# Optimization experiments

Hardware: AMD Instinct MI355X
Metric: run time of the kernel (lower is better)

The kernel has to match this reference:

```python
import jax, jax.numpy as jnp
import numpy as np

EPS = 1e-7
MIN_NORM = 1e-15
PROJ_EPS = 1e-5
NEG_SLOPE = 0.2
HEADS = 4


def artanh(x):
    return jnp.arctanh(jnp.clip(x, -1.0 + EPS, 1.0 - EPS))


def _norm(x):
    return jnp.clip(jnp.linalg.norm(x, axis=-1, keepdims=True), MIN_NORM)


def proj(x):
    # project onto Poincare ball (c=1)
    n = _norm(x)
    maxn = 1.0 - PROJ_EPS
    return jnp.where(n > maxn, x / n * maxn, x)


def expmap0(u):
    n = _norm(u)
    return jnp.tanh(n) * u / n


def logmap0(x):
    n = _norm(x)
    return artanh(n) * x / n


def mobius_add(x, y):
    x2 = jnp.sum(x * x, axis=-1, keepdims=True)
    y2 = jnp.sum(y * y, axis=-1, keepdims=True)
    xy = jnp.sum(x * y, axis=-1, keepdims=True)
    num = (1.0 + 2.0 * xy + y2) * x + (1.0 - x2) * y
    den = 1.0 + 2.0 * xy + x2 * y2
    return num / jnp.clip(den, MIN_NORM)


def pdist(x, y):
    # Poincare distance, c=1 -> [...,] scalar
    ma = mobius_add(-x, y)
    return 2.0 * artanh(jnp.linalg.norm(ma, axis=-1))


def mobius_scalar_mul(r, x):
    n = _norm(x)
    return jnp.tanh(r * artanh(n)) * x / n


def mobius_matvec(W, x):
    # x: [N,din], W: [dout,din]
    mx = x @ W.T
    n_x = _norm(x)
    n_mx = _norm(mx)
    return jnp.tanh(n_mx / n_x * artanh(n_x)) * mx / n_mx


def segment_softmax(logits, seg, num_segments):
    m = jax.ops.segment_max(logits, seg, num_segments=num_segments)
    m = jnp.where(jnp.isfinite(m), m, 0.0)
    e = jnp.exp(logits - m[seg])
    s = jax.ops.segment_sum(e, seg, num_segments=num_segments)
    return e / (s[seg] + 1e-16)


def setup_inputs() -> dict:
    N, E, D = 50000, 500000, 128
    H = HEADS
    Dh = D // H
    ks = jax.random.split(jax.random.key(0), 12)
    # edges without self-loops (reference re-adds them, mirroring remove/add_self_loops)
    src = jax.random.randint(ks[0], (E,), 0, N)
    off = jax.random.randint(ks[1], (E,), 1, N)
    dst = (src + off) % N
    edge_index = jnp.stack([src, dst]).astype(jnp.int32)
    x_e = 0.1 * jax.random.normal(ks[2], (N, D), dtype=jnp.float32)
    x_h = proj(expmap0(0.05 * jax.random.normal(ks[3], (N, D), dtype=jnp.float32)))
    sc = 1.0 / np.sqrt(D)
    W_e = sc * jax.random.normal(ks[4], (D, D), dtype=jnp.float32)
    b_lin_e = jnp.zeros((D,), jnp.float32)
    att_e = 0.1 * jax.random.normal(ks[5], (1, H, 2 * Dh), dtype=jnp.float32)
    b_e = jnp.zeros((D,), jnp.float32)
    W_h = sc * jax.random.normal(ks[6], (D, D), dtype=jnp.float32)
    b_lin_h = jnp.zeros((D,), jnp.float32)
    att_h = 0.1 * jax.random.normal(ks[7], (1, H, 2 * Dh), dtype=jnp.float32)
    b_h = jnp.zeros((D,), jnp.float32)
    att_hf = 0.1 * jax.random.normal(ks[8], (1, 1), dtype=jnp.float32)
    att_ef = 0.1 * jax.random.normal(ks[9], (1, 1), dtype=jnp.float32)
    return {"x_e": x_e, "x_h": x_h, "edge_index": edge_index,
            "W_e": W_e, "b_lin_e": b_lin_e, "att_e": att_e, "b_e": b_e,
            "W_h": W_h, "b_lin_h": b_lin_h, "att_h": att_h, "b_h": b_h,
            "att_hf": att_hf, "att_ef": att_ef}


def reference(x_e, x_h, edge_index, W_e, b_lin_e, att_e, b_e,
              W_h, b_lin_h, att_h, b_h, att_hf, att_ef):
    N, D = x_e.shape
    H = HEADS
    Dh = att_e.shape[-1] // 2
    loop = jnp.arange(N, dtype=edge_index.dtype)
    src = jnp.concatenate([edge_index[0], loop])  # j (source)
    dst = jnp.concatenate([edge_index[1], loop])  # i (target, softmax segment)

    # ---- Euclidean GAT branch (GATConv) ----
    xe = (x_e @ W_e.T + b_lin_e).reshape(N, H, Dh)
    a_i = jnp.sum(xe * att_e[:, :, :Dh], axis=-1)  # [N,H] target part
    a_j = jnp.sum(xe * att_e[:, :, Dh:], axis=-1)  # [N,H] source part
    alpha = jax.nn.leaky_relu(a_i[dst] + a_j[src], NEG_SLOPE)  # [E',H]
    alpha = segment_softmax(alpha, dst, N)
    agg = jax.ops.segment_sum(xe[src] * alpha[:, :, None], dst, num_segments=N)
    e_out = jax.nn.relu(agg.reshape(N, H * Dh) + b_e)

    # ---- Hyperbolic GAT branch (HGATConv with HypLinear) ----
    mv = proj(mobius_matvec(W_h, x_h))
    hb = proj(expmap0(b_lin_h))  # proj_tan0 is identity on Poincare ball
    xh = proj(mobius_add(mv, hb))  # [N,D] hyperbolic points (original_x)
    lx = logmap0(xh).reshape(N, H, Dh)
    hi = jnp.sum(lx * att_h[:, :, :Dh], axis=-1)
    hj = jnp.sum(lx * att_h[:, :, Dh:], axis=-1)
    alpha_h = hi[dst] + hj[src]  # [E',H]
    d = pdist(xh[dst], xh[src])  # [E'] hyperbolic edge distances
    d = segment_softmax(d, dst, N)[:, None]
    alpha_h = jax.nn.leaky_relu(alpha_h * d, NEG_SLOPE)
    alpha_h = segment_softmax(alpha_h, dst, N)
    agg_h = jax.ops.segment_sum(lx[src] * alpha_h[:, :, None], dst, num_segments=N)
    out_t = jax.nn.relu(agg_h.reshape(N, H * Dh) + b_h)  # tangent at origin
    h_out = proj(expmap0(out_t))

    # ---- HFusion: fuse Euclidean into hyperbolic ----
    ye = proj(expmap0(e_out))
    dist_f = (pdist(h_out, ye) * att_hf[0, 0])[:, None]  # [N,1]
    xe2 = proj(mobius_scalar_mul(dist_f, ye))
    h_fused = proj(mobius_add(h_out, xe2))

    # ---- EFusion: fuse hyperbolic into Euclidean ----
    lh = logmap0(h_out)
    de = (jnp.sum((lh - e_out) ** 2, axis=-1) * att_ef[0, 0])[:, None]
    e_fused = e_out + de * lh

    return jnp.stack([h_fused, e_fused])  # [2,N,D]
```

## Files before the change

kernel.cpp:

```cpp
#include <hip/hip_runtime.h>
#include <hip/hip_fp16.h>
#include <math.h>

typedef _Float16 h2 __attribute__((ext_vector_type(2)));
typedef _Float16 h8 __attribute__((ext_vector_type(8)));
typedef float f32x4 __attribute__((ext_vector_type(4)));

#define MAXN_BALL (1.0f - 1e-5f)
#define ART_CLIP  (1.0f - 1e-7f)
#define MAXD 48

__device__ __forceinline__ float f_rcp(float x)  { return __builtin_amdgcn_rcpf(x); }
__device__ __forceinline__ float f_exp(float x)  { return __expf(x); }
__device__ __forceinline__ float f_log(float x)  { return __logf(x); }
__device__ __forceinline__ float f_tanh(float x) {
    float ax = fabsf(x);
    float e = __expf(2.f * ax);
    float t = 1.f - 2.f * f_rcp(e + 1.f);
    return copysignf(t, x);
}
__device__ __forceinline__ float f_atanh(float x) {
    x = fminf(x, ART_CLIP);
    return 0.5f * f_log((1.f + x) * f_rcp(1.f - x));
}
__device__ __forceinline__ float leaky(float x) { return x > 0.0f ? x : 0.2f * x; }

union F4H8 { float4 f; h2 h[4]; };
union F2H4 { float2 f; h2 h[2]; };
union H8U  { h8 v; h2 h[4]; };
union H8F  { float4 f; h8 v; h2 h[4]; };

__device__ __forceinline__ h2 pk16(float x, float y) {
    union { decltype(__builtin_amdgcn_cvt_pkrtz(0.f, 0.f)) a; h2 b; } u;
    u.a = __builtin_amdgcn_cvt_pkrtz(x, y);
    return u.b;
}

__global__ __launch_bounds__(256) void k_wcvt(const float* __restrict__ W0,
                                              const float* __restrict__ W1,
                                              h2* __restrict__ W16) {
    int t = blockIdx.x * 256 + threadIdx.x;
    const float* W = (t < 2048) ? W0 : W1;
    int c = (t & 2047) * 8;
    float4 a = *(const float4*)(W + c);
    float4 b = *(const float4*)(W + c + 4);
    F4H8 u;
    u.h[0] = pk16(a.x, a.y); u.h[1] = pk16(a.z, a.w);
    u.h[2] = pk16(b.x, b.y); u.h[3] = pk16(b.z, b.w);
    *(float4*)&W16[(t >> 11) * 8192 + (c >> 1)] = u.f;
}

__global__ __launch_bounds__(256) void k_prep(const float* __restrict__ X0,
                                              const float* __restrict__ X1,
                                              const h2* __restrict__ W16,
                                              const float* __restrict__ bias0,
                                              h2* __restrict__ Y0,
                                              h2* __restrict__ Y1,
                                              int* __restrict__ counts,
                                              int N) {
    int t = threadIdx.x;
    if (blockIdx.y == 0) {
        int zi = blockIdx.x * 256 + t;
        if (zi < N) counts[zi] = 0;
    }
    int wv = t >> 6, l = t & 63;
    int rt = blockIdx.x * 4 + wv;
    if (rt * 16 >= N) return;
    int mat = blockIdx.y;
    const float* X = mat ? X1 : X0;
    const h2* Wbase = W16 + mat * 8192;
    h2* Y = mat ? Y1 : Y0;

    int lane16 = l & 15, quad = l >> 4;
    int r = rt * 16 + lane16;
    int rr = (r < N) ? r : (N - 1);
    const float* Xrow = &X[(size_t)rr * 128 + quad * 8];

    H8U bfr[4];
#pragma unroll
    for (int ks = 0; ks < 4; ++ks) {
        float4 xa = *(const float4*)(Xrow + ks * 32);
        float4 xb = *(const float4*)(Xrow + ks * 32 + 4);
        bfr[ks].h[0] = pk16(xa.x, xa.y); bfr[ks].h[1] = pk16(xa.z, xa.w);
        bfr[ks].h[2] = pk16(xb.x, xb.y); bfr[ks].h[3] = pk16(xb.z, xb.w);
    }

#pragma unroll
    for (int ct = 0; ct < 8; ++ct) {
        int o = ct * 16 + lane16;
        const h2* Wrow = &Wbase[o * 64 + quad * 4];
        f32x4 acc = {0.f, 0.f, 0.f, 0.f};
#pragma unroll
        for (int ks = 0; ks < 4; ++ks) {
            H8F a;
            a.f = *(const float4*)(Wrow + ks * 16);
            acc = __builtin_amdgcn_mfma_f32_16x16x32_f16(a.v, bfr[ks].v, acc, 0, 0, 0);
        }
        int obase = ct * 16 + quad * 4;
        float b0 = 0.f, b1 = 0.f, b2 = 0.f, b3 = 0.f;
        if (mat == 0) {
            b0 = bias0[obase]; b1 = bias0[obase + 1];
            b2 = bias0[obase + 2]; b3 = bias0[obase + 3];
        }
        if (r < N) {
            F2H4 u;
            u.h[0] = pk16(acc[0] + b0, acc[1] + b1);
            u.h[1] = pk16(acc[2] + b2, acc[3] + b3);
            *(float2*)&Y[(size_t)r * 64 + (obase >> 1)] = u.f;
        }
    }
}

__global__ __launch_bounds__(256) void k_node1_scatter(
        const h2* __restrict__ xe16, const float* __restrict__ x_h,
        const h2* __restrict__ mx16, h2* __restrict__ xh16,
        float* __restrict__ aux_j, float* __restrict__ aux_i,
        const float* __restrict__ att_e, const float* __restrict__ att_h,
        const float* __restrict__ b_lin_h,
        const int* __restrict__ ei, int* __restrict__ counts,
        int* __restrict__ srcs,
        int N, int E, int nblocks) {
    int t = threadIdx.x;
    int bx = blockIdx.x;
    if (bx >= nblocks) {
        int idx = (bx - nblocks) * 256 + t;
        if (idx < E + N) {
            int s, d;
            if (idx < E) { s = ei[idx]; d = ei[E + idx]; } else { s = d = idx - E; }
            int p = atomicAdd(&counts[d], 1);
            if (p < MAXD) srcs[d * MAXD + p] = s;
        }
        return;
    }
    int sl = t & 31, ni = t >> 5;
    int i = bx * 8 + ni;
    if (i >= N) return;
    int ht = sl >> 3, d0 = (sl & 7) * 4;

    F2H4 uxe; uxe.f = *(const float2*)&xe16[(size_t)i * 64 + 2 * sl];
    float4 xe4 = make_float4((float)uxe.h[0].x, (float)uxe.h[0].y,
                             (float)uxe.h[1].x, (float)uxe.h[1].y);
    float4 aeT = *(const float4*)&att_e[ht * 64 + d0];
    float4 aeS = *(const float4*)&att_e[ht * 64 + 32 + d0];
    float pi = xe4.x * aeT.x + xe4.y * aeT.y + xe4.z * aeT.z + xe4.w * aeT.w;
    float pj = xe4.x * aeS.x + xe4.y * aeS.y + xe4.z * aeS.z + xe4.w * aeS.w;
#pragma unroll
    for (int m = 1; m <= 4; m <<= 1) { pi += __shfl_xor(pi, m, 64); pj += __shfl_xor(pj, m, 64); }

    F2H4 umx; umx.f = *(const float2*)&mx16[(size_t)i * 64 + 2 * sl];
    float4 mx4 = make_float4((float)umx.h[0].x, (float)umx.h[0].y,
                             (float)umx.h[1].x, (float)umx.h[1].y);
    float4 xv4 = *(const float4*)&x_h[(size_t)i * 128 + 4 * sl];
    float4 bv4 = *(const float4*)&b_lin_h[4 * sl];
    float nx2  = xv4.x * xv4.x + xv4.y * xv4.y + xv4.z * xv4.z + xv4.w * xv4.w;
    float nmx2 = mx4.x * mx4.x + mx4.y * mx4.y + mx4.z * mx4.z + mx4.w * mx4.w;
    float nb2  = bv4.x * bv4.x + bv4.y * bv4.y + bv4.z * bv4.z + bv4.w * bv4.w;
    float dmb  = mx4.x * bv4.x + mx4.y * bv4.y + mx4.z * bv4.z + mx4.w * bv4.w;
#pragma unroll
    for (int m = 16; m >= 1; m >>= 1) {
        nx2 += __shfl_xor(nx2, m, 64); nmx2 += __shfl_xor(nmx2, m, 64);
        nb2 += __shfl_xor(nb2, m, 64); dmb  += __shfl_xor(dmb, m, 64);
    }

    float nxr = sqrtf(nx2),  nxc = fmaxf(nxr, 1e-15f);
    float nmxr = sqrtf(nmx2), nmxc = fmaxf(nmxr, 1e-15f);
    float tt = f_tanh(nmxc * f_rcp(nxc) * f_atanh(nxc));
    float c_m = tt * f_rcp(nmxc);
    float nmv = tt * (nmxr * f_rcp(nmxc));
    if (nmv > MAXN_BALL) { c_m *= MAXN_BALL / nmv; nmv = MAXN_BALL; }

    float nbr = sqrtf(nb2), nbc = fmaxf(nbr, 1e-15f);
    float tb = f_tanh(nbc);
    float c_b = tb * f_rcp(nbc);
    float nhb = tb * (nbr * f_rcp(nbc));
    if (nhb > MAXN_BALL) { c_b *= MAXN_BALL / nhb; nhb = MAXN_BALL; }

    float xy = c_m * c_b * dmb;
    float x2 = nmv * nmv, y2 = nhb * nhb;
    float den = fmaxf(1.f + 2.f * xy + x2 * y2, 1e-15f);
    float rden = f_rcp(den);
    float al = (1.f + 2.f * xy + y2) * c_m * rden;
    float be = (1.f - x2) * c_b * rden;
    float nr2 = al * al * nmx2 + 2.f * al * be * dmb + be * be * nb2;
    float nrr = sqrtf(nr2);
    if (nrr > MAXN_BALL) { float sc = MAXN_BALL / nrr; al *= sc; be *= sc; }
    float4 resv;
    resv.x = al * mx4.x + be * bv4.x; resv.y = al * mx4.y + be * bv4.y;
    resv.z = al * mx4.z + be * bv4.z; resv.w = al * mx4.w + be * bv4.w;
    F2H4 st;
    st.h[0] = pk16(resv.x, resv.y);
    st.h[1] = pk16(resv.z, resv.w);
    *(float2*)&xh16[(size_t)i * 64 + 2 * sl] = st.f;
    float4 rv = make_float4((float)st.h[0].x, (float)st.h[0].y,
                            (float)st.h[1].x, (float)st.h[1].y);

    float nr2r = rv.x * rv.x + rv.y * rv.y + rv.z * rv.z + rv.w * rv.w;
#pragma unroll
    for (int m = 16; m >= 1; m >>= 1) nr2r += __shfl_xor(nr2r, m, 64);
    float nrrr = sqrtf(nr2r);
    float nnc = fmaxf(nrrr, 1e-15f);
    float lam = f_atanh(nnc) * f_rcp(nnc);
    if (sl == 0) { aux_j[(size_t)i * 16 + 8] = lam; aux_j[(size_t)i * 16 + 9] = nr2r; }

    float4 lxv = make_float4(lam * rv.x, lam * rv.y, lam * rv.z, lam * rv.w);
    float4 ahT = *(const float4*)&att_h[ht * 64 + d0];
    float4 ahS = *(const float4*)&att_h[ht * 64 + 32 + d0];
    float qi = lxv.x * ahT.x + lxv.y * ahT.y + lxv.z * ahT.z + lxv.w * ahT.w;
    float qj = lxv.x * ahS.x + lxv.y * ahS.y + lxv.z * ahS.z + lxv.w * ahS.w;
#pragma unroll
    for (int m = 1; m <= 4; m <<= 1) { qi += __shfl_xor(qi, m, 64); qj += __shfl_xor(qj, m, 64); }
    if ((sl & 7) == 0) {
        aux_j[(size_t)i * 16 + ht] = qj;
        aux_j[(size_t)i * 16 + 4 + ht] = pj;
        aux_i[(size_t)i * 8 + ht] = qi;
        aux_i[(size_t)i * 8 + 4 + ht] = pi;
    }
}

__global__ __launch_bounds__(256) void k_node_final(
    const h2* __restrict__ xh16, const float* __restrict__ aux_j,
    const float* __restrict__ aux_i, const h2* __restrict__ xe16,
    const int* __restrict__ counts, const int* __restrict__ srcs,
    const float* __restrict__ b_e, const float* __restrict__ b_h,
    const float* __restrict__ att_hf, const float* __restrict__ att_ef,
    float* __restrict__ out, int N) {
    __shared__ int   s_src_all[8][MAXD];
    __shared__ float s_d_all[8][MAXD];
    __shared__ float s_ah_all[8][MAXD * 4];
    __shared__ float s_ae_all[8][MAXD * 4];

    int t = threadIdx.x;
    int sl = t & 31, ni = t >> 5;
    int i = blockIdx.x * 8 + ni;
    if (i >= N) return;
    int*   s_src = s_src_all[ni];
    float* s_d   = s_d_all[ni];
    float* s_ah  = s_ah_all[ni];
    float* s_ae  = s_ae_all[ni];

    int deg = counts[i];
    if (deg > MAXD) deg = MAXD;
    if (sl < deg)      s_src[sl]      = srcs[i * MAXD + sl];
    if (sl + 32 < deg) s_src[sl + 32] = srcs[i * MAXD + sl + 32];

    float x2i = aux_j[(uint32_t)i * 16u + 9u];
    {
        int g = sl & 7, sub = sl >> 3;
        uint32_t goff = (uint32_t)(g * 8);
        const h2* xi = &xh16[(uint32_t)i * 64u + goff];
        F4H8 us0, us1;
        us0.f = *(const float4*)xi;
        us1.f = *(const float4*)(xi + 4);
        for (int p = 0; p * 4 < deg; ++p) {
            int e = p * 4 + sub;
            bool act = e < deg;
            float dot = 0.f;
            int j = 0;
            if (act) {
                j = s_src[e];
                uint32_t oj = (uint32_t)j * 64u + goff;
                F4H8 ua, ub;
                ua.f = *(const float4*)&xh16[oj];
                ub.f = *(const float4*)&xh16[oj + 4u];
#pragma unroll
                for (int k = 0; k < 4; ++k) dot = __builtin_amdgcn_fdot2(ua.h[k], us0.h[k], dot, false);
#pragma unroll
                for (int k = 0; k < 4; ++k) dot = __builtin_amdgcn_fdot2(ub.h[k], us1.h[k], dot, false);
            }
            dot += __shfl_xor(dot, 1, 64);
            dot += __shfl_xor(dot, 2, 64);
            dot += __shfl_xor(dot, 4, 64);
            if (act && g == 0) {
                float y2 = aux_j[(uint32_t)j * 16u + 9u];
                float xy = dot;
                float A = 1.f - 2.f * xy + y2;
                float B = 1.f - x2i;
                float den = fmaxf(1.f - 2.f * xy + x2i * y2, 1e-15f);
                float num2 = fmaxf(A * A * x2i - 2.f * A * B * xy + B * B * y2, 0.f);
                float nma = fminf(sqrtf(num2) * f_rcp(den), ART_CLIP);
                s_d[e] = f_log((1.f + nma) * f_rcp(1.f - nma));
            }
        }
    }

    float eA = (sl < deg)      ? f_exp(s_d[sl])      : 0.f;
    float eB = (sl + 32 < deg) ? f_exp(s_d[sl + 32]) : 0.f;
    float ssum = eA + eB;
#pragma unroll
    for (int m = 16; m >= 1; m >>= 1) ssum += __shfl_xor(ssum, m, 64);
    float dinv = f_rcp(ssum + 1e-16f);

    float4 hi4 = *(const float4*)&aux_i[(uint32_t)i * 8u];
    float4 ai4 = *(const float4*)&aux_i[(uint32_t)i * 8u + 4u];
    float4 vh_s[2], ve_s[2];
    float lam_s[2] = {0.f, 0.f};
    float4 sh = make_float4(0.f, 0.f, 0.f, 0.f), se = sh;
#pragma unroll
    for (int s = 0; s < 2; ++s) {
        int e = sl + 32 * s;
        if (e < deg) {
            int j = s_src[e];
            float ds = (s ? eB : eA) * dinv;
            uint32_t oj = (uint32_t)j * 16u;
            float4 hj4 = *(const float4*)&aux_j[oj];
            float4 aj4 = *(const float4*)&aux_j[oj + 4u];
            lam_s[s] = aux_j[oj + 8u];
            float4 vh, ve;
            vh.x = f_exp(leaky((hi4.x + hj4.x) * ds));
            vh.y = f_exp(leaky((hi4.y + hj4.y) * ds));
            vh.z = f_exp(leaky((hi4.z + hj4.z) * ds));
            vh.w = f_exp(leaky((hi4.w + hj4.w) * ds));
            ve.x = f_exp(leaky(ai4.x + aj4.x));
            ve.y = f_exp(leaky(ai4.y + aj4.y));
            ve.z = f_exp(leaky(ai4.z + aj4.z));
            ve.w = f_exp(leaky(ai4.w + aj4.w));
            vh_s[s] = vh; ve_s[s] = ve;
            sh.x += vh.x; sh.y += vh.y; sh.z += vh.z; sh.w += vh.w;
            se.x += ve.x; se.y += ve.y; se.z += ve.z; se.w += ve.w;
        }
    }
#pragma unroll
    for (int m = 16; m >= 1; m >>= 1) {
        sh.x += __shfl_xor(sh.x, m, 64); sh.y += __shfl_xor(sh.y, m, 64);
        sh.z += __shfl_xor(sh.z, m, 64); sh.w += __shfl_xor(sh.w, m, 64);
        se.x += __shfl_xor(se.x, m, 64); se.y += __shfl_xor(se.y, m, 64);
        se.z += __shfl_xor(se.z, m, 64); se.w += __shfl_xor(se.w, m, 64);
    }
    float4 rh = make_float4(f_rcp(sh.x + 1e-16f), f_rcp(sh.y + 1e-16f),
                            f_rcp(sh.z + 1e-16f), f_rcp(sh.w + 1e-16f));
    float4 re = make_float4(f_rcp(se.x + 1e-16f), f_rcp(se.y + 1e-16f),
                            f_rcp(se.z + 1e-16f), f_rcp(se.w + 1e-16f));
#pragma unroll
    for (int s = 0; s < 2; ++s) {
        int e = sl + 32 * s;
        if (e < deg) {
            float lamj = lam_s[s];
            float4 vh = vh_s[s], ve = ve_s[s];
            vh.x *= rh.x * lamj; vh.y *= rh.y * lamj; vh.z *= rh.z * lamj; vh.w *= rh.w * lamj;
            ve.x *= re.x; ve.y *= re.y; ve.z *= re.z; ve.w *= re.w;
            *(float4*)&s_ah[e * 4] = vh;
            *(float4*)&s_ae[e * 4] = ve;
        }
    }

    int hq = sl >> 3;
    uint32_t dsl = 2u * (uint32_t)sl;
    float4 aE = make_float4(0.f, 0.f, 0.f, 0.f), aH = aE;
    int e = 0;
    for (; e + 3 < deg; e += 4) {
        int j0 = s_src[e], j1 = s_src[e + 1], j2 = s_src[e + 2], j3 = s_src[e + 3];
        uint32_t o0 = (uint32_t)j0 * 64u + dsl, o1 = (uint32_t)j1 * 64u + dsl;
        uint32_t o2 = (uint32_t)j2 * 64u + dsl, o3 = (uint32_t)j3 * 64u + dsl;
        F2H4 ux0, uh0, ux1, uh1, ux2, uh2, ux3, uh3;
        ux0.f = *(const float2*)&xe16[o0]; uh0.f = *(const float2*)&xh16[o0];
        ux1.f = *(const float2*)&xe16[o1]; uh1.f = *(const float2*)&xh16[o1];
        ux2.f = *(const float2*)&xe16[o2]; uh2.f = *(const float2*)&xh16[o2];
        ux3.f = *(const float2*)&xe16[o3]; uh3.f = *(const float2*)&xh16[o3];
        float we0 = s_ae[e * 4 + hq],       wh0 = s_ah[e * 4 + hq];
        float we1 = s_ae[(e + 1) * 4 + hq], wh1 = s_ah[(e + 1) * 4 + hq];
        float we2 = s_ae[(e + 2) * 4 + hq], wh2 = s_ah[(e + 2) * 4 + hq];
        float we3 = s_ae[(e + 3) * 4 + hq], wh3 = s_ah[(e + 3) * 4 + hq];
        aE.x += we0 * (float)ux0.h[0].x + we1 * (float)ux1.h[0].x;
        aE.y += we0 * (float)ux0.h[0].y + we1 * (float)ux1.h[0].y;
        aE.z += we0 * (float)ux0.h[1].x + we1 * (float)ux1.h[1].x;
        aE.w += we0 * (float)ux0.h[1].y + we1 * (float)ux1.h[1].y;
        aH.x += wh0 * (float)uh0.h[0].x + wh1 * (float)uh1.h[0].x;
        aH.y += wh0 * (float)uh0.h[0].y + wh1 * (float)uh1.h[0].y;
        aH.z += wh0 * (float)uh0.h[1].x + wh1 * (float)uh1.h[1].x;
        aH.w += wh0 * (float)uh0.h[1].y + wh1 * (float)uh1.h[1].y;
        aE.x += we2 * (float)ux2.h[0].x + we3 * (float)ux3.h[0].x;
        aE.y += we2 * (float)ux2.h[0].y + we3 * (float)ux3.h[0].y;
        aE.z += we2 * (float)ux2.h[1].x + we3 * (float)ux3.h[1].x;
        aE.w += we2 * (float)ux2.h[1].y + we3 * (float)ux3.h[1].y;
        aH.x += wh2 * (float)uh2.h[0].x + wh3 * (float)uh3.h[0].x;
        aH.y += wh2 * (float)uh2.h[0].y + wh3 * (float)uh3.h[0].y;
        aH.z += wh2 * (float)uh2.h[1].x + wh3 * (float)uh3.h[1].x;
        aH.w += wh2 * (float)uh2.h[1].y + wh3 * (float)uh3.h[1].y;
    }
    for (; e + 1 < deg; e += 2) {
        int j0 = s_src[e], j1 = s_src[e + 1];
        uint32_t o0 = (uint32_t)j0 * 64u + dsl, o1 = (uint32_t)j1 * 64u + dsl;
        F2H4 ux0, uh0, ux1, uh1;
        ux0.f = *(const float2*)&xe16[o0]; uh0.f = *(const float2*)&xh16[o0];
        ux1.f = *(const float2*)&xe16[o1]; uh1.f = *(const float2*)&xh16[o1];
        float we0 = s_ae[e * 4 + hq], wh0 = s_ah[e * 4 + hq];
        float we1 = s_ae[(e + 1) * 4 + hq], wh1 = s_ah[(e + 1) * 4 + hq];
        aE.x += we0 * (float)ux0.h[0].x + we1 * (float)ux1.h[0].x;
        aE.y += we0 * (float)ux0.h[0].y + we1 * (float)ux1.h[0].y;
        aE.z += we0 * (float)ux0.h[1].x + we1 * (float)ux1.h[1].x;
        aE.w += we0 * (float)ux0.h[1].y + we1 * (float)ux1.h[1].y;
        aH.x += wh0 * (float)uh0.h[0].x + wh1 * (float)uh1.h[0].x;
        aH.y += wh0 * (float)uh0.h[0].y + wh1 * (float)uh1.h[0].y;
        aH.z += wh0 * (float)uh0.h[1].x + wh1 * (float)uh1.h[1].x;
        aH.w += wh0 * (float)uh0.h[1].y + wh1 * (float)uh1.h[1].y;
    }
    if (e < deg) {
        int j = s_src[e];
        uint32_t oj = (uint32_t)j * 64u + dsl;
        F2H4 ux, uh;
        ux.f = *(const float2*)&xe16[oj];
        uh.f = *(const float2*)&xh16[oj];
        float we = s_ae[e * 4 + hq], wh = s_ah[e * 4 + hq];
        aE.x += we * (float)ux.h[0].x; aE.y += we * (float)ux.h[0].y;
        aE.z += we * (float)ux.h[1].x; aE.w += we * (float)ux.h[1].y;
        aH.x += wh * (float)uh.h[0].x; aH.y += wh * (float)uh.h[0].y;
        aH.z += wh * (float)uh.h[1].x; aH.w += wh * (float)uh.h[1].y;
    }

    float4 be4 = *(const float4*)&b_e[4 * sl];
    float4 bh4 = *(const float4*)&b_h[4 * sl];
    float4 eo, ot;
    eo.x = fmaxf(aE.x + be4.x, 0.f); eo.y = fmaxf(aE.y + be4.y, 0.f);
    eo.z = fmaxf(aE.z + be4.z, 0.f); eo.w = fmaxf(aE.w + be4.w, 0.f);
    ot.x = fmaxf(aH.x + bh4.x, 0.f); ot.y = fmaxf(aH.y + bh4.y, 0.f);
    ot.z = fmaxf(aH.z + bh4.z, 0.f); ot.w = fmaxf(aH.w + bh4.w, 0.f);
    float n2  = ot.x * ot.x + ot.y * ot.y + ot.z * ot.z + ot.w * ot.w;
    float ne2 = eo.x * eo.x + eo.y * eo.y + eo.z * eo.z + eo.w * eo.w;
    float dot3 = ot.x * eo.x + ot.y * eo.y + ot.z * eo.z + ot.w * eo.w;
#pragma unroll
    for (int m = 16; m >= 1; m >>= 1) {
        n2 += __shfl_xor(n2, m, 64); ne2 += __shfl_xor(ne2, m, 64); dot3 += __shfl_xor(dot3, m, 64);
    }

    float n_raw = sqrtf(n2), n_c = fmaxf(n_raw, 1e-15f);
    float th = f_tanh(n_c);
    float c_h = th * f_rcp(n_c);
    float nh = th * (n_raw * f_rcp(n_c));
    if (nh > MAXN_BALL) { c_h *= MAXN_BALL / nh; nh = MAXN_BALL; }

    float nE_raw = sqrtf(ne2), nE_c = fmaxf(nE_raw, 1e-15f);
    float tE = f_tanh(nE_c);
    float c_e = tE * f_rcp(nE_c);
    float ny = tE * (nE_raw * f_rcp(nE_c));
    if (ny > MAXN_BALL) { c_e *= MAXN_BALL / ny; ny = MAXN_BALL; }

    float xyv = c_h * c_e * dot3;
    float x2f = nh * nh, y2f = ny * ny;
    float A = 1.f - 2.f * xyv + y2f, B = 1.f - x2f;
    float den = fmaxf(1.f - 2.f * xyv + x2f * y2f, 1e-15f);
    float num2 = fmaxf(A * A * x2f - 2.f * A * B * xyv + B * B * y2f, 0.f);
    float nma = fminf(sqrtf(num2) * f_rcp(den), ART_CLIP);
    float distf = f_log((1.f + nma) * f_rcp(1.f - nma)) * att_hf[0];
    float nyc = fmaxf(ny, 1e-15f);
    float s1 = f_tanh(distf * f_atanh(nyc)) * f_rcp(nyc);
    float nxe2 = fabsf(s1) * ny;
    if (nxe2 > MAXN_BALL) { s1 *= MAXN_BALL / nxe2; nxe2 = MAXN_BALL; }
    float xy2 = s1 * xyv;
    float y22 = nxe2 * nxe2;
    float rden2 = f_rcp(fmaxf(1.f + 2.f * xy2 + x2f * y22, 1e-15f));
    float alpha = (1.f + 2.f * xy2 + y22) * rden2 * c_h;
    float beta  = (1.f - x2f) * s1 * rden2 * c_e;
    float nf2 = alpha * alpha * n2 + 2.f * alpha * beta * dot3 + beta * beta * ne2;
    float nf = sqrtf(nf2);
    if (nf > MAXN_BALL) { float sc = MAXN_BALL / nf; alpha *= sc; beta *= sc; }

    float nhc = fmaxf(nh, 1e-15f);
    float gam = f_atanh(nhc) * f_rcp(nhc) * c_h;
    float de2 = gam * gam * n2 - 2.f * gam * dot3 + ne2;
    float dg = de2 * att_ef[0] * gam;

    float4 o1;
    o1.x = alpha * ot.x + beta * eo.x; o1.y = alpha * ot.y + beta * eo.y;
    o1.z = alpha * ot.z + beta * eo.z; o1.w = alpha * ot.w + beta * eo.w;
    *(float4*)&out[(size_t)i * 128 + 4 * sl] = o1;
    float4 o2;
    o2.x = eo.x + dg * ot.x; o2.y = eo.y + dg * ot.y;
    o2.z = eo.z + dg * ot.z; o2.w = eo.w + dg * ot.w;
    *(float4*)&out[(size_t)N * 128 + (size_t)i * 128 + 4 * sl] = o2;
}

extern "C" void kernel_launch(void* const* d_in, const int* in_sizes, int n_in,
                              void* d_out, int out_size, void* d_ws, size_t ws_size,
                              hipStream_t stream) {
    const float* x_e      = (const float*)d_in[0];
    const float* x_h      = (const float*)d_in[1];
    const int*   ei       = (const int*)d_in[2];
    const float* W_e      = (const float*)d_in[3];
    const float* b_lin_e  = (const float*)d_in[4];
    const float* att_e    = (const float*)d_in[5];
    const float* b_e      = (const float*)d_in[6];
    const float* W_h      = (const float*)d_in[7];
    const float* b_lin_h  = (const float*)d_in[8];
    const float* att_h    = (const float*)d_in[9];
    const float* b_h      = (const float*)d_in[10];
    const float* att_hf   = (const float*)d_in[11];
    const float* att_ef   = (const float*)d_in[12];

    int N = in_sizes[0] / 128;
    int E = in_sizes[2] / 2;
    int EN = E + N;

    char* ws = (char*)d_ws;
    size_t off = 0;
    auto alloc = [&](size_t bytes) -> void* {
        void* p = ws + off;
        off = (off + bytes + 255) & ~(size_t)255;
        return p;
    };
    h2*    W16   = (h2*)alloc((size_t)2 * 8192 * 4);
    h2*    xe16  = (h2*)alloc((size_t)N * 128 * 2);
    h2*    mx16  = (h2*)alloc((size_t)N * 128 * 2);
    h2*    xh16  = (h2*)alloc((size_t)N * 128 * 2);
    float* aux_j = (float*)alloc((size_t)N * 16 * 4);
    float* aux_i = (float*)alloc((size_t)N * 8 * 4);
    int*   counts= (int*)alloc((size_t)N * 4);
    int*   srcs  = (int*)alloc((size_t)N * MAXD * 4);

    k_wcvt<<<16, 256, 0, stream>>>(W_e, W_h, W16);

    int rtiles = (N + 15) / 16;
    int rblocks = (rtiles + 3) / 4;
    dim3 pgrid(rblocks, 2);
    k_prep<<<pgrid, 256, 0, stream>>>(x_e, x_h, W16, b_lin_e,
                                      xe16, mx16, counts, N);

    int nblocks = (N + 7) / 8;
    int eblocks = (EN + 255) / 256;
    k_node1_scatter<<<nblocks + eblocks, 256, 0, stream>>>(
        xe16, x_h, mx16, xh16, aux_j, aux_i,
        att_e, att_h, b_lin_h, ei, counts, srcs, N, E, nblocks);

    int fblocks = (N + 7) / 8;
    k_node_final<<<fblocks, 256, 0, stream>>>(xh16, aux_j, aux_i, xe16,
                                              counts, srcs, b_e, b_h, att_hf, att_ef,
                                              (float*)d_out, N);
}
```

Baseline: 272.6 us.

## Move edge scatter into GEMM kernel and process two row tiles per wave

Zeroing of the per-node edge counters moves into the weight-conversion kernel. The edge-bucketing scatter moves from the node kernel into the projection GEMM kernel as a third grid slice, so the atomic scatter runs alongside the MFMA work. Each wave in the GEMM now handles 32 rows, reusing each loaded weight fragment for two MFMA chains. This shortens the node kernel and overlaps latency-bound atomics with compute, at the cost of more registers per wave and an oversized grid in which idle GEMM slice blocks exit early.

```diff
diff --git a/kernel.cpp b/kernel.cpp
--- a/kernel.cpp
+++ b/kernel.cpp
@@ -38,16 +38,24 @@
 
 __global__ __launch_bounds__(256) void k_wcvt(const float* __restrict__ W0,
                                               const float* __restrict__ W1,
-                                              h2* __restrict__ W16) {
-    int t = blockIdx.x * 256 + threadIdx.x;
-    const float* W = (t < 2048) ? W0 : W1;
-    int c = (t & 2047) * 8;
+                                              h2* __restrict__ W16,
+                                              int* __restrict__ counts,
+                                              int N, int cblocks) {
+    int b = blockIdx.x, t = threadIdx.x;
+    if (b < cblocks) {
+        int zi = b * 256 + t;
+        if (zi < N) counts[zi] = 0;
+        return;
+    }
+    int tw = (b - cblocks) * 256 + t;
+    const float* W = (tw < 2048) ? W0 : W1;
+    int c = (tw & 2047) * 8;
     float4 a = *(const float4*)(W + c);
-    float4 b = *(const float4*)(W + c + 4);
+    float4 bb = *(const float4*)(W + c + 4);
     F4H8 u;
-    u.h[0] = pk16(a.x, a.y); u.h[1] = pk16(a.z, a.w);
-    u.h[2] = pk16(b.x, b.y); u.h[3] = pk16(b.z, b.w);
-    *(float4*)&W16[(t >> 11) * 8192 + (c >> 1)] = u.f;
+    u.h[0] = pk16(a.x, a.y);  u.h[1] = pk16(a.z, a.w);
+    u.h[2] = pk16(bb.x, bb.y); u.h[3] = pk16(bb.z, bb.w);
+    *(float4*)&W16[(tw >> 11) * 8192 + (c >> 1)] = u.f;
 }
 
 __global__ __launch_bounds__(256) void k_prep(const float* __restrict__ X0,
@@ -56,74 +64,13 @@
                                               const float* __restrict__ bias0,
                                               h2* __restrict__ Y0,
                                               h2* __restrict__ Y1,
+                                              const int* __restrict__ ei,
                                               int* __restrict__ counts,
-                                              int N) {
+                                              int* __restrict__ srcs,
+                                              int N, int E) {
     int t = threadIdx.x;
-    if (blockIdx.y == 0) {
-        int zi = blockIdx.x * 256 + t;
-        if (zi < N) counts[zi] = 0;
-    }
-    int wv = t >> 6, l = t & 63;
-    int rt = blockIdx.x * 4 + wv;
-    if (rt * 16 >= N) return;
-    int mat = blockIdx.y;
-    const float* X = mat ? X1 : X0;
-    const h2* Wbase = W16 + mat * 8192;
-    h2* Y = mat ? Y1 : Y0;
-
-    int lane16 = l & 15, quad = l >> 4;
-    int r = rt * 16 + lane16;
-    int rr = (r < N) ? r : (N - 1);
-    const float* Xrow = &X[(size_t)rr * 128 + quad * 8];
-
-    H8U bfr[4];
-#pragma unroll
-    for (int ks = 0; ks < 4; ++ks) {
-        float4 xa = *(const float4*)(Xrow + ks * 32);
-        float4 xb = *(const float4*)(Xrow + ks * 32 + 4);
-        bfr[ks].h[0] = pk16(xa.x, xa.y); bfr[ks].h[1] = pk16(xa.z, xa.w);
-        bfr[ks].h[2] = pk16(xb.x, xb.y); bfr[ks].h[3] = pk16(xb.z, xb.w);
-    }
-
-#pragma unroll
-    for (int ct = 0; ct < 8; ++ct) {
-        int o = ct * 16 + lane16;
-        const h2* Wrow = &Wbase[o * 64 + quad * 4];
-        f32x4 acc = {0.f, 0.f, 0.f, 0.f};
-#pragma unroll
-        for (int ks = 0; ks < 4; ++ks) {
-            H8F a;
-            a.f = *(const float4*)(Wrow + ks * 16);
-            acc = __builtin_amdgcn_mfma_f32_16x16x32_f16(a.v, bfr[ks].v, acc, 0, 0, 0);
-        }
-        int obase = ct * 16 + quad * 4;
-        float b0 = 0.f, b1 = 0.f, b2 = 0.f, b3 = 0.f;
-        if (mat == 0) {
-            b0 = bias0[obase]; b1 = bias0[obase + 1];
-            b2 = bias0[obase + 2]; b3 = bias0[obase + 3];
-        }
-        if (r < N) {
-            F2H4 u;
-            u.h[0] = pk16(acc[0] + b0, acc[1] + b1);
-            u.h[1] = pk16(acc[2] + b2, acc[3] + b3);
-            *(float2*)&Y[(size_t)r * 64 + (obase >> 1)] = u.f;
-        }
-    }
-}
-
-__global__ __launch_bounds__(256) void k_node1_scatter(
-        const h2* __restrict__ xe16, const float* __restrict__ x_h,
-        const h2* __restrict__ mx16, h2* __restrict__ xh16,
-        float* __restrict__ aux_j, float* __restrict__ aux_i,
-        const float* __restrict__ att_e, const float* __restrict__ att_h,
-        const float* __restrict__ b_lin_h,
-        const int* __restrict__ ei, int* __restrict__ counts,
-        int* __restrict__ srcs,
-        int N, int E, int nblocks) {
-    int t = threadIdx.x;
-    int bx = blockIdx.x;
-    if (bx >= nblocks) {
-        int idx = (bx - nblocks) * 256 + t;
+    if (blockIdx.y == 2) {
+        int idx = blockIdx.x * 256 + t;
         if (idx < E + N) {
             int s, d;
             if (idx < E) { s = ei[idx]; d = ei[E + idx]; } else { s = d = idx - E; }
@@ -132,8 +79,77 @@
         }
         return;
     }
+    int wv = t >> 6, l = t & 63;
+    int rt = blockIdx.x * 4 + wv;
+    if (rt * 32 >= N) return;
+    int mat = blockIdx.y;
+    const float* X = mat ? X1 : X0;
+    const h2* Wbase = W16 + mat * 8192;
+    h2* Y = mat ? Y1 : Y0;
+
+    int lane16 = l & 15, quad = l >> 4;
+    int r0 = rt * 32 + lane16, r1 = r0 + 16;
+    int rr0 = (r0 < N) ? r0 : (N - 1);
+    int rr1 = (r1 < N) ? r1 : (N - 1);
+    const float* Xrow0 = &X[(size_t)rr0 * 128 + quad * 8];
+    const float* Xrow1 = &X[(size_t)rr1 * 128 + quad * 8];
+
+    H8U b0r[4], b1r[4];
+#pragma unroll
+    for (int ks = 0; ks < 4; ++ks) {
+        float4 xa = *(const float4*)(Xrow0 + ks * 32);
+        float4 xb = *(const float4*)(Xrow0 + ks * 32 + 4);
+        b0r[ks].h[0] = pk16(xa.x, xa.y); b0r[ks].h[1] = pk16(xa.z, xa.w);
+        b0r[ks].h[2] = pk16(xb.x, xb.y); b0r[ks].h[3] = pk16(xb.z, xb.w);
+        float4 ya = *(const float4*)(Xrow1 + ks * 32);
+        float4 yb = *(const float4*)(Xrow1 + ks * 32 + 4);
+        b1r[ks].h[0] = pk16(ya.x, ya.y); b1r[ks].h[1] = pk16(ya.z, ya.w);
+        b1r[ks].h[2] = pk16(yb.x, yb.y); b1r[ks].h[3] = pk16(yb.z, yb.w);
+    }
+
+#pragma unroll
+    for (int ct = 0; ct < 8; ++ct) {
+        int o = ct * 16 + lane16;
+        const h2* Wrow = &Wbase[o * 64 + quad * 4];
+        f32x4 acc0 = {0.f, 0.f, 0.f, 0.f};
+        f32x4 acc1 = {0.f, 0.f, 0.f, 0.f};
+#pragma unroll
+        for (int ks = 0; ks < 4; ++ks) {
+            H8F a;
+            a.f = *(const float4*)(Wrow + ks * 16);
+            acc0 = __builtin_amdgcn_mfma_f32_16x16x32_f16(a.v, b0r[ks].v, acc0, 0, 0, 0);
+            acc1 = __builtin_amdgcn_mfma_f32_16x16x32_f16(a.v, b1r[ks].v, acc1, 0, 0, 0);
+        }
+        int obase = ct * 16 + quad * 4;
+        float c0 = 0.f, c1 = 0.f, c2 = 0.f, c3 = 0.f;
+        if (mat == 0) {
+            c0 = bias0[obase]; c1 = bias0[obase + 1];
+            c2 = bias0[obase + 2]; c3 = bias0[obase + 3];
+        }
+        if (r0 < N) {
+            F2H4 u;
+            u.h[0] = pk16(acc0[0] + c0, acc0[1] + c1);
+            u.h[1] = pk16(acc0[2] + c2, acc0[3] + c3);
+            *(float2*)&Y[(size_t)r0 * 64 + (obase >> 1)] = u.f;
+        }
+        if (r1 < N) {
+            F2H4 u;
+            u.h[0] = pk16(acc1[0] + c0, acc1[1] + c1);
+            u.h[1] = pk16(acc1[2] + c2, acc1[3] + c3);
+            *(float2*)&Y[(size_t)r1 * 64 + (obase >> 1)] = u.f;
+        }
+    }
+}
+
+__global__ __launch_bounds__(256) void k_node1(
+        const h2* __restrict__ xe16, const float* __restrict__ x_h,
+        const h2* __restrict__ mx16, h2* __restrict__ xh16,
+        float* __restrict__ aux_j, float* __restrict__ aux_i,
+        const float* __restrict__ att_e, const float* __restrict__ att_h,
+        const float* __restrict__ b_lin_h, int N) {
+    int t = threadIdx.x;
     int sl = t & 31, ni = t >> 5;
-    int i = bx * 8 + ni;
+    int i = blockIdx.x * 8 + ni;
     if (i >= N) return;
     int ht = sl >> 3, d0 = (sl & 7) * 4;
 
@@ -506,19 +522,21 @@
     int*   counts= (int*)alloc((size_t)N * 4);
     int*   srcs  = (int*)alloc((size_t)N * MAXD * 4);
 
-    k_wcvt<<<16, 256, 0, stream>>>(W_e, W_h, W16);
-
-    int rtiles = (N + 15) / 16;
+    int cblocks = (N + 255) / 256;
+    k_wcvt<<<cblocks + 16, 256, 0, stream>>>(W_e, W_h, W16, counts, N, cblocks);
+
+    int rtiles = (N + 31) / 32;
     int rblocks = (rtiles + 3) / 4;
-    dim3 pgrid(rblocks, 2);
+    int eblocks = (EN + 255) / 256;
+    int gx = rblocks > eblocks ? rblocks : eblocks;
+    dim3 pgrid(gx, 3);
     k_prep<<<pgrid, 256, 0, stream>>>(x_e, x_h, W16, b_lin_e,
-                                      xe16, mx16, counts, N);
+                                      xe16, mx16, ei, counts, srcs, N, E);
 
     int nblocks = (N + 7) / 8;
-    int eblocks = (EN + 255) / 256;
-    k_node1_scatter<<<nblocks + eblocks, 256, 0, stream>>>(
+    k_node1<<<nblocks, 256, 0, stream>>>(
         xe16, x_h, mx16, xh16, aux_j, aux_i,
-        att_e, att_h, b_lin_h, ei, counts, srcs, N, E, nblocks);
+        att_e, att_h, b_lin_h, N);
 
     int fblocks = (N + 7) / 8;
     k_node_final<<<fblocks, 256, 0, stream>>>(xh16, aux_j, aux_i, xe16,
```

Result: faster. 249.6 us (-8.4%).

## Fuse both MFMA projections with node-level hyperbolic prep and edge scatter

Applied to the files above, without the earlier changes.

Merges the two-matrix projection kernel and the per-node hyperbolic/attention kernel into one. Each wave now computes both GEMMs for its 16 rows and does the Mobius matvec, bias add, projection and attention dot products straight from MFMA accumulators in registers. This removes the fp16 mx16 intermediate and its round trip through global memory, plus one launch. The zeroing of counts moves into the weight-convert kernel so the edge scatter can run as the second grid row of the fused kernel. In exchange, register pressure rises from holding eight accumulator tiles and bias vectors, and per-head reductions now use cross-quad shuffles.

```diff
diff --git a/kernel.cpp b/kernel.cpp
--- a/kernel.cpp
+++ b/kernel.cpp
@@ -38,44 +38,54 @@
 
 __global__ __launch_bounds__(256) void k_wcvt(const float* __restrict__ W0,
                                               const float* __restrict__ W1,
-                                              h2* __restrict__ W16) {
-    int t = blockIdx.x * 256 + threadIdx.x;
-    const float* W = (t < 2048) ? W0 : W1;
-    int c = (t & 2047) * 8;
+                                              h2* __restrict__ W16,
+                                              int* __restrict__ counts,
+                                              int N, int cblocks) {
+    int b = blockIdx.x, t = threadIdx.x;
+    if (b < cblocks) {
+        int zi = b * 256 + t;
+        if (zi < N) counts[zi] = 0;
+        return;
+    }
+    int tw = (b - cblocks) * 256 + t;
+    const float* W = (tw < 2048) ? W0 : W1;
+    int c = (tw & 2047) * 8;
     float4 a = *(const float4*)(W + c);
-    float4 b = *(const float4*)(W + c + 4);
+    float4 bb = *(const float4*)(W + c + 4);
     F4H8 u;
-    u.h[0] = pk16(a.x, a.y); u.h[1] = pk16(a.z, a.w);
-    u.h[2] = pk16(b.x, b.y); u.h[3] = pk16(b.z, b.w);
-    *(float4*)&W16[(t >> 11) * 8192 + (c >> 1)] = u.f;
-}
-
-__global__ __launch_bounds__(256) void k_prep(const float* __restrict__ X0,
-                                              const float* __restrict__ X1,
-                                              const h2* __restrict__ W16,
-                                              const float* __restrict__ bias0,
-                                              h2* __restrict__ Y0,
-                                              h2* __restrict__ Y1,
-                                              int* __restrict__ counts,
-                                              int N) {
+    u.h[0] = pk16(a.x, a.y);  u.h[1] = pk16(a.z, a.w);
+    u.h[2] = pk16(bb.x, bb.y); u.h[3] = pk16(bb.z, bb.w);
+    *(float4*)&W16[(tw >> 11) * 8192 + (c >> 1)] = u.f;
+}
+
+__global__ __launch_bounds__(256) void k_prep_fused(
+        const float* __restrict__ x_e, const float* __restrict__ x_h,
+        const h2* __restrict__ W16,
+        const float* __restrict__ b_lin_e, const float* __restrict__ b_lin_h,
+        const float* __restrict__ att_e, const float* __restrict__ att_h,
+        h2* __restrict__ xe16, h2* __restrict__ xh16,
+        float* __restrict__ aux_j, float* __restrict__ aux_i,
+        const int* __restrict__ ei, int* __restrict__ counts,
+        int* __restrict__ srcs, int N, int E) {
     int t = threadIdx.x;
-    if (blockIdx.y == 0) {
-        int zi = blockIdx.x * 256 + t;
-        if (zi < N) counts[zi] = 0;
+    if (blockIdx.y == 1) {
+        int idx = blockIdx.x * 256 + t;
+        if (idx < E + N) {
+            int s, d;
+            if (idx < E) { s = ei[idx]; d = ei[E + idx]; } else { s = d = idx - E; }
+            int p = atomicAdd(&counts[d], 1);
+            if (p < MAXD) srcs[d * MAXD + p] = s;
+        }
+        return;
     }
     int wv = t >> 6, l = t & 63;
     int rt = blockIdx.x * 4 + wv;
     if (rt * 16 >= N) return;
-    int mat = blockIdx.y;
-    const float* X = mat ? X1 : X0;
-    const h2* Wbase = W16 + mat * 8192;
-    h2* Y = mat ? Y1 : Y0;
-
     int lane16 = l & 15, quad = l >> 4;
     int r = rt * 16 + lane16;
     int rr = (r < N) ? r : (N - 1);
-    const float* Xrow = &X[(size_t)rr * 128 + quad * 8];
-
+
+    const float* Xrow = &x_e[(size_t)rr * 128 + quad * 8];
     H8U bfr[4];
 #pragma unroll
     for (int ks = 0; ks < 4; ++ks) {
@@ -84,11 +94,10 @@
         bfr[ks].h[0] = pk16(xa.x, xa.y); bfr[ks].h[1] = pk16(xa.z, xa.w);
         bfr[ks].h[2] = pk16(xb.x, xb.y); bfr[ks].h[3] = pk16(xb.z, xb.w);
     }
-
+    float pi[4] = {0.f, 0.f, 0.f, 0.f}, pj[4] = {0.f, 0.f, 0.f, 0.f};
 #pragma unroll
     for (int ct = 0; ct < 8; ++ct) {
-        int o = ct * 16 + lane16;
-        const h2* Wrow = &Wbase[o * 64 + quad * 4];
+        const h2* Wrow = &W16[(ct * 16 + lane16) * 64 + quad * 4];
         f32x4 acc = {0.f, 0.f, 0.f, 0.f};
 #pragma unroll
         for (int ks = 0; ks < 4; ++ks) {
@@ -97,69 +106,56 @@
             acc = __builtin_amdgcn_mfma_f32_16x16x32_f16(a.v, bfr[ks].v, acc, 0, 0, 0);
         }
         int obase = ct * 16 + quad * 4;
-        float b0 = 0.f, b1 = 0.f, b2 = 0.f, b3 = 0.f;
-        if (mat == 0) {
-            b0 = bias0[obase]; b1 = bias0[obase + 1];
-            b2 = bias0[obase + 2]; b3 = bias0[obase + 3];
-        }
-        if (r < N) {
-            F2H4 u;
-            u.h[0] = pk16(acc[0] + b0, acc[1] + b1);
-            u.h[1] = pk16(acc[2] + b2, acc[3] + b3);
-            *(float2*)&Y[(size_t)r * 64 + (obase >> 1)] = u.f;
-        }
-    }
-}
-
-__global__ __launch_bounds__(256) void k_node1_scatter(
-        const h2* __restrict__ xe16, const float* __restrict__ x_h,
-        const h2* __restrict__ mx16, h2* __restrict__ xh16,
-        float* __restrict__ aux_j, float* __restrict__ aux_i,
-        const float* __restrict__ att_e, const float* __restrict__ att_h,
-        const float* __restrict__ b_lin_h,
-        const int* __restrict__ ei, int* __restrict__ counts,
-        int* __restrict__ srcs,
-        int N, int E, int nblocks) {
-    int t = threadIdx.x;
-    int bx = blockIdx.x;
-    if (bx >= nblocks) {
-        int idx = (bx - nblocks) * 256 + t;
-        if (idx < E + N) {
-            int s, d;
-            if (idx < E) { s = ei[idx]; d = ei[E + idx]; } else { s = d = idx - E; }
-            int p = atomicAdd(&counts[d], 1);
-            if (p < MAXD) srcs[d * MAXD + p] = s;
-        }
-        return;
-    }
-    int sl = t & 31, ni = t >> 5;
-    int i = bx * 8 + ni;
-    if (i >= N) return;
-    int ht = sl >> 3, d0 = (sl & 7) * 4;
-
-    F2H4 uxe; uxe.f = *(const float2*)&xe16[(size_t)i * 64 + 2 * sl];
-    float4 xe4 = make_float4((float)uxe.h[0].x, (float)uxe.h[0].y,
-                             (float)uxe.h[1].x, (float)uxe.h[1].y);
-    float4 aeT = *(const float4*)&att_e[ht * 64 + d0];
-    float4 aeS = *(const float4*)&att_e[ht * 64 + 32 + d0];
-    float pi = xe4.x * aeT.x + xe4.y * aeT.y + xe4.z * aeT.z + xe4.w * aeT.w;
-    float pj = xe4.x * aeS.x + xe4.y * aeS.y + xe4.z * aeS.z + xe4.w * aeS.w;
-#pragma unroll
-    for (int m = 1; m <= 4; m <<= 1) { pi += __shfl_xor(pi, m, 64); pj += __shfl_xor(pj, m, 64); }
-
-    F2H4 umx; umx.f = *(const float2*)&mx16[(size_t)i * 64 + 2 * sl];
-    float4 mx4 = make_float4((float)umx.h[0].x, (float)umx.h[0].y,
-                             (float)umx.h[1].x, (float)umx.h[1].y);
-    float4 xv4 = *(const float4*)&x_h[(size_t)i * 128 + 4 * sl];
-    float4 bv4 = *(const float4*)&b_lin_h[4 * sl];
-    float nx2  = xv4.x * xv4.x + xv4.y * xv4.y + xv4.z * xv4.z + xv4.w * xv4.w;
-    float nmx2 = mx4.x * mx4.x + mx4.y * mx4.y + mx4.z * mx4.z + mx4.w * mx4.w;
-    float nb2  = bv4.x * bv4.x + bv4.y * bv4.y + bv4.z * bv4.z + bv4.w * bv4.w;
-    float dmb  = mx4.x * bv4.x + mx4.y * bv4.y + mx4.z * bv4.z + mx4.w * bv4.w;
-#pragma unroll
-    for (int m = 16; m >= 1; m >>= 1) {
+        float4 bb = *(const float4*)&b_lin_e[obase];
+        F2H4 u;
+        u.h[0] = pk16(acc[0] + bb.x, acc[1] + bb.y);
+        u.h[1] = pk16(acc[2] + bb.z, acc[3] + bb.w);
+        if (r < N) *(float2*)&xe16[(size_t)r * 64 + (obase >> 1)] = u.f;
+        float4 xe4 = make_float4((float)u.h[0].x, (float)u.h[0].y,
+                                 (float)u.h[1].x, (float)u.h[1].y);
+        int hd = ct >> 1, w0 = (ct & 1) * 16 + quad * 4;
+        float4 aT = *(const float4*)&att_e[hd * 64 + w0];
+        float4 aS = *(const float4*)&att_e[hd * 64 + 32 + w0];
+        pi[hd] += xe4.x * aT.x + xe4.y * aT.y + xe4.z * aT.z + xe4.w * aT.w;
+        pj[hd] += xe4.x * aS.x + xe4.y * aS.y + xe4.z * aS.z + xe4.w * aS.w;
+    }
+
+    const float* Xrow1 = &x_h[(size_t)rr * 128 + quad * 8];
+    float nx2 = 0.f;
+#pragma unroll
+    for (int ks = 0; ks < 4; ++ks) {
+        float4 xa = *(const float4*)(Xrow1 + ks * 32);
+        float4 xb = *(const float4*)(Xrow1 + ks * 32 + 4);
+        nx2 += xa.x * xa.x + xa.y * xa.y + xa.z * xa.z + xa.w * xa.w
+             + xb.x * xb.x + xb.y * xb.y + xb.z * xb.z + xb.w * xb.w;
+        bfr[ks].h[0] = pk16(xa.x, xa.y); bfr[ks].h[1] = pk16(xa.z, xa.w);
+        bfr[ks].h[2] = pk16(xb.x, xb.y); bfr[ks].h[3] = pk16(xb.z, xb.w);
+    }
+    f32x4 mx[8];
+    float4 bh[8];
+    float nmx2 = 0.f, dmb = 0.f, nb2 = 0.f;
+#pragma unroll
+    for (int ct = 0; ct < 8; ++ct) {
+        const h2* Wrow = &W16[8192 + (ct * 16 + lane16) * 64 + quad * 4];
+        f32x4 acc = {0.f, 0.f, 0.f, 0.f};
+#pragma unroll
+        for (int ks = 0; ks < 4; ++ks) {
+            H8F a;
+            a.f = *(const float4*)(Wrow + ks * 16);
+            acc = __builtin_amdgcn_mfma_f32_16x16x32_f16(a.v, bfr[ks].v, acc, 0, 0, 0);
+        }
+        mx[ct] = acc;
+        int obase = ct * 16 + quad * 4;
+        float4 bv = *(const float4*)&b_lin_h[obase];
+        bh[ct] = bv;
+        nmx2 += acc[0] * acc[0] + acc[1] * acc[1] + acc[2] * acc[2] + acc[3] * acc[3];
+        dmb  += acc[0] * bv.x + acc[1] * bv.y + acc[2] * bv.z + acc[3] * bv.w;
+        nb2  += bv.x * bv.x + bv.y * bv.y + bv.z * bv.z + bv.w * bv.w;
+    }
+#pragma unroll
+    for (int m = 16; m <= 32; m <<= 1) {
         nx2 += __shfl_xor(nx2, m, 64); nmx2 += __shfl_xor(nmx2, m, 64);
-        nb2 += __shfl_xor(nb2, m, 64); dmb  += __shfl_xor(dmb, m, 64);
+        dmb += __shfl_xor(dmb, m, 64); nb2  += __shfl_xor(nb2, m, 64);
     }
 
     float nxr = sqrtf(nx2),  nxc = fmaxf(nxr, 1e-15f);
@@ -184,36 +180,55 @@
     float nr2 = al * al * nmx2 + 2.f * al * be * dmb + be * be * nb2;
     float nrr = sqrtf(nr2);
     if (nrr > MAXN_BALL) { float sc = MAXN_BALL / nrr; al *= sc; be *= sc; }
-    float4 resv;
-    resv.x = al * mx4.x + be * bv4.x; resv.y = al * mx4.y + be * bv4.y;
-    resv.z = al * mx4.z + be * bv4.z; resv.w = al * mx4.w + be * bv4.w;
-    F2H4 st;
-    st.h[0] = pk16(resv.x, resv.y);
-    st.h[1] = pk16(resv.z, resv.w);
-    *(float2*)&xh16[(size_t)i * 64 + 2 * sl] = st.f;
-    float4 rv = make_float4((float)st.h[0].x, (float)st.h[0].y,
-                            (float)st.h[1].x, (float)st.h[1].y);
-
-    float nr2r = rv.x * rv.x + rv.y * rv.y + rv.z * rv.z + rv.w * rv.w;
-#pragma unroll
-    for (int m = 16; m >= 1; m >>= 1) nr2r += __shfl_xor(nr2r, m, 64);
+
+    float nr2r = 0.f;
+    float sT[4] = {0.f, 0.f, 0.f, 0.f}, sS[4] = {0.f, 0.f, 0.f, 0.f};
+#pragma unroll
+    for (int ct = 0; ct < 8; ++ct) {
+        float4 resv;
+        resv.x = al * mx[ct][0] + be * bh[ct].x;
+        resv.y = al * mx[ct][1] + be * bh[ct].y;
+        resv.z = al * mx[ct][2] + be * bh[ct].z;
+        resv.w = al * mx[ct][3] + be * bh[ct].w;
+        F2H4 u;
+        u.h[0] = pk16(resv.x, resv.y);
+        u.h[1] = pk16(resv.z, resv.w);
+        int obase = ct * 16 + quad * 4;
+        if (r < N) *(float2*)&xh16[(size_t)r * 64 + (obase >> 1)] = u.f;
+        float4 rv = make_float4((float)u.h[0].x, (float)u.h[0].y,
+                                (float)u.h[1].x, (float)u.h[1].y);
+        nr2r += rv.x * rv.x + rv.y * rv.y + rv.z * rv.z + rv.w * rv.w;
+        int hd = ct >> 1, w0 = (ct & 1) * 16 + quad * 4;
+        float4 hT = *(const float4*)&att_h[hd * 64 + w0];
+        float4 hS = *(const float4*)&att_h[hd * 64 + 32 + w0];
+        sT[hd] += rv.x * hT.x + rv.y * hT.y + rv.z * hT.z + rv.w * hT.w;
+        sS[hd] += rv.x * hS.x + rv.y * hS.y + rv.z * hS.z + rv.w * hS.w;
+    }
+#pragma unroll
+    for (int m = 16; m <= 32; m <<= 1) {
+        nr2r += __shfl_xor(nr2r, m, 64);
+#pragma unroll
+        for (int hd = 0; hd < 4; ++hd) {
+            pi[hd] += __shfl_xor(pi[hd], m, 64);
+            pj[hd] += __shfl_xor(pj[hd], m, 64);
+            sT[hd] += __shfl_xor(sT[hd], m, 64);
+            sS[hd] += __shfl_xor(sS[hd], m, 64);
+        }
+    }
     float nrrr = sqrtf(nr2r);
     float nnc = fmaxf(nrrr, 1e-15f);
     float lam = f_atanh(nnc) * f_rcp(nnc);
-    if (sl == 0) { aux_j[(size_t)i * 16 + 8] = lam; aux_j[(size_t)i * 16 + 9] = nr2r; }
-
-    float4 lxv = make_float4(lam * rv.x, lam * rv.y, lam * rv.z, lam * rv.w);
-    float4 ahT = *(const float4*)&att_h[ht * 64 + d0];
-    float4 ahS = *(const float4*)&att_h[ht * 64 + 32 + d0];
-    float qi = lxv.x * ahT.x + lxv.y * ahT.y + lxv.z * ahT.z + lxv.w * ahT.w;
-    float qj = lxv.x * ahS.x + lxv.y * ahS.y + lxv.z * ahS.z + lxv.w * ahS.w;
-#pragma unroll
-    for (int m = 1; m <= 4; m <<= 1) { qi += __shfl_xor(qi, m, 64); qj += __shfl_xor(qj, m, 64); }
-    if ((sl & 7) == 0) {
-        aux_j[(size_t)i * 16 + ht] = qj;
-        aux_j[(size_t)i * 16 + 4 + ht] = pj;
-        aux_i[(size_t)i * 8 + ht] = qi;
-        aux_i[(size_t)i * 8 + 4 + ht] = pi;
+
+    if (quad == 0 && r < N) {
+        float4 qj4 = make_float4(lam * sS[0], lam * sS[1], lam * sS[2], lam * sS[3]);
+        float4 pj4 = make_float4(pj[0], pj[1], pj[2], pj[3]);
+        *(float4*)&aux_j[(size_t)r * 16]     = qj4;
+        *(float4*)&aux_j[(size_t)r * 16 + 4] = pj4;
+        *(float2*)&aux_j[(size_t)r * 16 + 8] = make_float2(lam, nr2r);
+        float4 qi4 = make_float4(lam * sT[0], lam * sT[1], lam * sT[2], lam * sT[3]);
+        float4 pi4 = make_float4(pi[0], pi[1], pi[2], pi[3]);
+        *(float4*)&aux_i[(size_t)r * 8]     = qi4;
+        *(float4*)&aux_i[(size_t)r * 8 + 4] = pi4;
     }
 }
 
@@ -499,26 +514,23 @@
     };
     h2*    W16   = (h2*)alloc((size_t)2 * 8192 * 4);
     h2*    xe16  = (h2*)alloc((size_t)N * 128 * 2);
-    h2*    mx16  = (h2*)alloc((size_t)N * 128 * 2);
     h2*    xh16  = (h2*)alloc((size_t)N * 128 * 2);
     float* aux_j = (float*)alloc((size_t)N * 16 * 4);
     float* aux_i = (float*)alloc((size_t)N * 8 * 4);
     int*   counts= (int*)alloc((size_t)N * 4);
     int*   srcs  = (int*)alloc((size_t)N * MAXD * 4);
 
-    k_wcvt<<<16, 256, 0, stream>>>(W_e, W_h, W16);
+    int cblocks = (N + 255) / 256;
+    k_wcvt<<<cblocks + 16, 256, 0, stream>>>(W_e, W_h, W16, counts, N, cblocks);
 
     int rtiles = (N + 15) / 16;
     int rblocks = (rtiles + 3) / 4;
-    dim3 pgrid(rblocks, 2);
-    k_prep<<<pgrid, 256, 0, stream>>>(x_e, x_h, W16, b_lin_e,
-                                      xe16, mx16, counts, N);
-
-    int nblocks = (N + 7) / 8;
     int eblocks = (EN + 255) / 256;
-    k_node1_scatter<<<nblocks + eblocks, 256, 0, stream>>>(
-        xe16, x_h, mx16, xh16, aux_j, aux_i,
-        att_e, att_h, b_lin_h, ei, counts, srcs, N, E, nblocks);
+    int gx = rblocks > eblocks ? rblocks : eblocks;
+    dim3 pgrid(gx, 2);
+    k_prep_fused<<<pgrid, 256, 0, stream>>>(x_e, x_h, W16, b_lin_e, b_lin_h,
+                                            att_e, att_h, xe16, xh16, aux_j, aux_i,
+                                            ei, counts, srcs, N, E);
 
     int fblocks = (N + 7) / 8;
     k_node_final<<<fblocks, 256, 0, stream>>>(xh16, aux_j, aux_i, xe16,
```

Result: faster. 252.7 us (-7.3%).
